# Optimization experiments

Measured on AMD Instinct MI355X. Metric: run time of the kernel, lower is better.

The kernel has to match this reference:

```python
import jax, jax.numpy as jnp
import numpy as np

B, NPG, C = 256, 256, 256  # graphs, nodes-per-graph, in_channels
MAX_LEN = 500


def _sinusoid_pe(max_len, c):
    pos = np.arange(max_len, dtype=np.float32)[:, None]
    div = np.exp(np.arange(0, c, 2, dtype=np.float32) * (-np.log(10000.0) / c))
    pe = np.zeros((max_len, c), np.float32)
    pe[:, 0::2] = np.sin(pos * div)
    pe[:, 1::2] = np.cos(pos * div)
    return jnp.asarray(pe)


def setup_inputs() -> dict:
    key = jax.random.key(0)
    ks = jax.random.split(key, 8)
    N = B * NPG
    x = jax.random.normal(ks[0], (N, C), jnp.float32)
    batch = jnp.repeat(jnp.arange(B, dtype=jnp.int32), NPG)
    # every other atom in each graph is an N/O atom -> 128 per graph
    on_index = (jnp.arange(B, dtype=jnp.int32)[:, None] * NPG
                + jnp.arange(0, NPG, 2, dtype=jnp.int32)[None, :]).reshape(-1)
    W1 = jax.random.normal(ks[1], (C, 256), jnp.float32) / np.sqrt(C)
    b1 = jnp.zeros((256,), jnp.float32)
    W2 = jax.random.normal(ks[2], (256, 128), jnp.float32) / np.sqrt(256.0)
    b2 = jnp.zeros((128,), jnp.float32)
    W3 = jax.random.normal(ks[3], (128, 64), jnp.float32) / np.sqrt(128.0)
    b3 = jnp.zeros((64,), jnp.float32)
    w_atom = jax.random.normal(ks[4], (64,), jnp.float32) / 8.0
    return {"x": x, "pe": _sinusoid_pe(MAX_LEN, C), "W1": W1, "b1": b1,
            "W2": W2, "b2": b2, "W3": W3, "b3": b3, "w_atom": w_atom,
            "batch": batch, "on_index": on_index, "ratio": 16}


def _lrelu(z):
    return jnp.where(z > 0, z, 0.1 * z)


def reference(x, pe, W1, b1, W2, b2, W3, b3, w_atom, batch, on_index, ratio):
    N = x.shape[0]
    bsz = int(batch[-1]) + 1
    num_nodes = jax.ops.segment_sum(jnp.ones_like(batch), batch, num_segments=bsz)
    cum = jnp.concatenate([jnp.zeros((1,), batch.dtype), jnp.cumsum(num_nodes)[:-1]])
    n = int(num_nodes.max())  # max_num_nodes
    idx_in_graph = jnp.arange(N, dtype=batch.dtype) - cum[batch]
    # positional encoding (dropout = identity in eval)
    xp = x + pe[idx_in_graph]
    # scoring MLP
    h = _lrelu(xp @ W1 + b1)
    h = _lrelu(h @ W2 + b2)
    h = _lrelu(h @ W3 + b3)
    score = jnp.tanh((h * w_atom).sum(-1) / jnp.linalg.norm(w_atom))
    # dense-pack scores into [bsz, n] padded with -inf, sort descending per row
    dense_idx = jnp.arange(N, dtype=batch.dtype) - cum[batch] + batch * n
    dense = jnp.full((bsz * n,), jnp.finfo(x.dtype).min, x.dtype).at[dense_idx].set(score)
    order = jnp.argsort(-dense.reshape(bsz, n), axis=-1)       # perm within row
    ranks = jnp.argsort(order, axis=-1)                         # inverse perm
    pos_in_perm = (jnp.arange(bsz)[:, None] * n + ranks).reshape(-1)
    # positions (in the flattened perm) of N/O atoms, sorted -> grouped per graph
    on_par = dense_idx[on_index]                                # padded/parallel ids
    indices = jnp.sort(pos_in_perm[on_par])
    m = on_index.shape[0] // bsz                                # N/O atoms per graph (uniform here)
    k = min(int(ratio), m)                                      # k = min(ratio, on_num)
    pre_mask = (jnp.arange(bsz)[:, None] * m + jnp.arange(k)[None, :]).reshape(-1)
    mask = indices[pre_mask]
    # map padded indices back to global node ids (subtract cumulative void counts)
    void = n - num_nodes
    cum_void = jnp.concatenate([jnp.zeros((1,), batch.dtype), jnp.cumsum(void)[:-1]])
    perm_flat = (order + (jnp.arange(bsz) * n - cum_void)[:, None]).reshape(-1)
    perm = perm_flat[mask]
    x_top = (xp[perm] * score[perm][:, None]).reshape(bsz, int(ratio), -1)
    return (x_top, perm, score[on_index], on_index)
```

## Files before the change

### kernel.cpp

```cpp
#include <hip/hip_runtime.h>
#include <hip/hip_bf16.h>


typedef __attribute__((ext_vector_type(8))) short short8v;
typedef __attribute__((ext_vector_type(4))) float float4v;

#define W1P_OFF 0
#define W2P_OFF 131072
#define W3P_OFF 196608
#define NORM_OFF 212992

static __device__ __forceinline__ float lrelu(float z) { return z > 0.0f ? z : 0.1f * z; }

static __device__ __forceinline__ unsigned f2bfu(float f) {
    union { float f; unsigned u; } v; v.f = f;
    const unsigned r = v.u + 0x7FFFu + ((v.u >> 16) & 1u);
    return r >> 16;
}
static __device__ __forceinline__ short f2bf(float f) { return (short)f2bfu(f); }

static __device__ __forceinline__ int sw_off(int row, int chunk, int within) {
    return row * 256 + ((chunk ^ (row & 7)) << 3) + within;
}

__global__ __launch_bounds__(256) void pack_kernel(
    const float* __restrict__ W1, const float* __restrict__ W2,
    const float* __restrict__ W3, const float* __restrict__ wa,
    short* __restrict__ ws, float* __restrict__ ws_norm)
{
    const int u = blockIdx.x * 256 + threadIdx.x;
    if (u >= 13312) {
        if (u < 13312 + 64) {
            const int l = u - 13312;
            float w = wa[l];
            float p = w * w;
            #pragma unroll
            for (int s = 1; s < 64; s <<= 1) p += __shfl_xor(p, s);
            if (l == 0) ws_norm[0] = sqrtf(p);
        }
        return;
    }
    const float* W; int N, unitBase, uu;
    short* dst;
    if (u < 8192)       { W = W1; N = 256; uu = u;         dst = ws + (W1P_OFF/2); unitBase = 8; }
    else if (u < 12288) { W = W2; N = 128; uu = u - 8192;  dst = ws + (W2P_OFF/2); unitBase = 8; }
    else                { W = W3; N = 64;  uu = u - 12288; dst = ws + (W3P_OFF/2); unitBase = 4; }
    const int perNt = unitBase * 64;
    const int nt   = uu / perNt;
    const int rem  = uu % perNt;
    const int ks   = rem / 64;
    const int lane = rem % 64;
    const int q = lane >> 4;
    const int n = nt * 16 + (lane & 15);
    short8v frag;
    #pragma unroll
    for (int j = 0; j < 8; ++j) {
        const int k = ks * 32 + q * 8 + j;
        frag[j] = f2bf(W[(size_t)k * N + n]);
    }
    *(short8v*)(dst + (size_t)uu * 8) = frag;
}

__global__ __launch_bounds__(1024, 4) void fused_mlp_topk_kernel(
    const float* __restrict__ x, const float* __restrict__ pe,
    const float* __restrict__ b1, const float* __restrict__ b2,
    const float* __restrict__ b3, const float* __restrict__ w_atom,
    const int* __restrict__ on_index, const short* __restrict__ ws_pack,
    const float* __restrict__ ws_norm,
    float* __restrict__ out_perm, float* __restrict__ out_xtop,
    float* __restrict__ out_score, float* __restrict__ out_onidx)
{
    __shared__ __align__(16) short XP[128 * 256];
    __shared__ __align__(16) short H1[128 * 256];
    __shared__ float PART[128][5];
    __shared__ float SC[128];
    __shared__ int   sel_node[16];
    __shared__ float sel_sc[16];

    const int t    = threadIdx.x;
    const int g    = blockIdx.x;
    const int m0   = g * 128;
    const int wid  = t >> 6;
    const int lane = t & 63;
    const int q = lane >> 4;
    const int c = lane & 15;

    const short* W1p = ws_pack + (W1P_OFF / 2);
    const short* W2p = ws_pack + (W2P_OFF / 2);
    const short* W3p = ws_pack + (W3P_OFF / 2);

    #pragma unroll
    for (int i = 0; i < 4; ++i) {
        const int u = t + i * 1024;
        const int r = u >> 5;
        const int ck = u & 31;
        const int k = ck << 3;
        const int node = on_index[m0 + r];
        const float4 xa = *(const float4*)(x + (size_t)node * 256 + k);
        const float4 xb = *(const float4*)(x + (size_t)node * 256 + k + 4);
        const float4 pa = *(const float4*)(pe + (size_t)(node & 255) * 256 + k);
        const float4 pb = *(const float4*)(pe + (size_t)(node & 255) * 256 + k + 4);
        short8v s;
        s[0] = f2bf(xa.x + pa.x); s[1] = f2bf(xa.y + pa.y);
        s[2] = f2bf(xa.z + pa.z); s[3] = f2bf(xa.w + pa.w);
        s[4] = f2bf(xb.x + pb.x); s[5] = f2bf(xb.y + pb.y);
        s[6] = f2bf(xb.z + pb.z); s[7] = f2bf(xb.w + pb.w);
        *(short8v*)(&XP[sw_off(r, ck, 0)]) = s;
    }
    __syncthreads();

    {
        const int mg = wid >> 3;
        const int ng = wid & 7;
        const int r0 = mg * 64;
        float4v acc[2][4];
        #pragma unroll
        for (int gg = 0; gg < 2; ++gg) {
            const float4 bb = *(const float4*)(b1 + (ng * 2 + gg) * 16 + q * 4);
            #pragma unroll
            for (int mt = 0; mt < 4; ++mt)
                acc[gg][mt] = (float4v){bb.x, bb.y, bb.z, bb.w};
        }
        #pragma unroll
        for (int ks = 0; ks < 8; ++ks) {
            const short8v w0 = *(const short8v*)(W1p + ((size_t)((ng * 2 + 0) * 8 + ks) * 64 + lane) * 8);
            const short8v w1 = *(const short8v*)(W1p + ((size_t)((ng * 2 + 1) * 8 + ks) * 64 + lane) * 8);
            #pragma unroll
            for (int mt = 0; mt < 4; ++mt) {
                const short8v a = *(const short8v*)(&XP[sw_off(r0 + mt * 16 + c, ks * 4 + q, 0)]);
                acc[0][mt] = __builtin_amdgcn_mfma_f32_16x16x32_bf16(w0, a, acc[0][mt], 0, 0, 0);
                acc[1][mt] = __builtin_amdgcn_mfma_f32_16x16x32_bf16(w1, a, acc[1][mt], 0, 0, 0);
            }
        }
        #pragma unroll
        for (int gg = 0; gg < 2; ++gg) {
            const int nbase = (ng * 2 + gg) * 16 + q * 4;
            const int chunk = nbase >> 3;
            const int within = nbase & 7;
            #pragma unroll
            for (int mt = 0; mt < 4; ++mt) {
                const int m = r0 + mt * 16 + c;
                uint2 dd;
                dd.x = f2bfu(lrelu(acc[gg][mt][0])) | (f2bfu(lrelu(acc[gg][mt][1])) << 16);
                dd.y = f2bfu(lrelu(acc[gg][mt][2])) | (f2bfu(lrelu(acc[gg][mt][3])) << 16);
                *(uint2*)(&H1[sw_off(m, chunk, within)]) = dd;
            }
        }
    }
    __syncthreads();

    {
        const int mg = wid >> 2;
        const int ng = wid & 3;
        const int r0 = mg * 32;
        float4v acc[2][2];
        #pragma unroll
        for (int gg = 0; gg < 2; ++gg) {
            const float4 bb = *(const float4*)(b2 + (ng * 2 + gg) * 16 + q * 4);
            #pragma unroll
            for (int mt = 0; mt < 2; ++mt)
                acc[gg][mt] = (float4v){bb.x, bb.y, bb.z, bb.w};
        }
        #pragma unroll
        for (int ks = 0; ks < 8; ++ks) {
            const short8v w0 = *(const short8v*)(W2p + ((size_t)((ng * 2 + 0) * 8 + ks) * 64 + lane) * 8);
            const short8v w1 = *(const short8v*)(W2p + ((size_t)((ng * 2 + 1) * 8 + ks) * 64 + lane) * 8);
            #pragma unroll
            for (int mt = 0; mt < 2; ++mt) {
                const short8v a = *(const short8v*)(&H1[sw_off(r0 + mt * 16 + c, ks * 4 + q, 0)]);
                acc[0][mt] = __builtin_amdgcn_mfma_f32_16x16x32_bf16(w0, a, acc[0][mt], 0, 0, 0);
                acc[1][mt] = __builtin_amdgcn_mfma_f32_16x16x32_bf16(w1, a, acc[1][mt], 0, 0, 0);
            }
        }
        #pragma unroll
        for (int gg = 0; gg < 2; ++gg) {
            const int nbase = (ng * 2 + gg) * 16 + q * 4;
            const int chunk = nbase >> 3;
            const int within = nbase & 7;
            #pragma unroll
            for (int mt = 0; mt < 2; ++mt) {
                const int m = r0 + mt * 16 + c;
                uint2 dd;
                dd.x = f2bfu(lrelu(acc[gg][mt][0])) | (f2bfu(lrelu(acc[gg][mt][1])) << 16);
                dd.y = f2bfu(lrelu(acc[gg][mt][2])) | (f2bfu(lrelu(acc[gg][mt][3])) << 16);
                *(uint2*)(&XP[sw_off(m, chunk, within)]) = dd;
            }
        }
    }
    __syncthreads();

    {
        const int nt  = wid & 3;
        const int mt0 = (wid >> 2) * 2;
        float4v acc[2];
        const float4 bb = *(const float4*)(b3 + nt * 16 + q * 4);
        acc[0] = (float4v){bb.x, bb.y, bb.z, bb.w};
        acc[1] = (float4v){bb.x, bb.y, bb.z, bb.w};
        #pragma unroll
        for (int ks = 0; ks < 4; ++ks) {
            const short8v w = *(const short8v*)(W3p + ((size_t)(nt * 4 + ks) * 64 + lane) * 8);
            const short8v a0 = *(const short8v*)(&XP[sw_off((mt0 + 0) * 16 + c, ks * 4 + q, 0)]);
            const short8v a1 = *(const short8v*)(&XP[sw_off((mt0 + 1) * 16 + c, ks * 4 + q, 0)]);
            acc[0] = __builtin_amdgcn_mfma_f32_16x16x32_bf16(w, a0, acc[0], 0, 0, 0);
            acc[1] = __builtin_amdgcn_mfma_f32_16x16x32_bf16(w, a1, acc[1], 0, 0, 0);
        }
        const float4 wv = *(const float4*)(w_atom + nt * 16 + q * 4);
        #pragma unroll
        for (int mt = 0; mt < 2; ++mt) {
            float p = lrelu(acc[mt][0]) * wv.x + lrelu(acc[mt][1]) * wv.y
                    + lrelu(acc[mt][2]) * wv.z + lrelu(acc[mt][3]) * wv.w;
            p += __shfl_xor(p, 16);
            p += __shfl_xor(p, 32);
            if (q == 0) PART[(mt0 + mt) * 16 + c][nt] = p;
        }
    }
    __syncthreads();

    if (t < 128) {
        const float sum = PART[t][0] + PART[t][1] + PART[t][2] + PART[t][3];
        const float sc = tanhf(sum / ws_norm[0]);
        SC[t] = sc;
        out_score[m0 + t] = sc;
        out_onidx[m0 + t] = (float)on_index[m0 + t];
    }
    __syncthreads();

    if (t < 128) {
        const float sj = SC[t];
        int rank = 0;
        for (int i = 0; i < 128; ++i) {
            const float si = SC[i];
            rank += (si > sj) || (si == sj && i < t);
        }
        if (rank < 16) {
            const int node = on_index[m0 + t];
            sel_node[rank] = node;
            sel_sc[rank]   = sj;
            out_perm[g * 16 + rank] = (float)node;
        }
    }
    __syncthreads();

    #pragma unroll
    for (int i = 0; i < 4; ++i) {
        const int idx = t + i * 1024;
        const int k   = idx >> 8;
        const int col = idx & 255;
        const int node = sel_node[k];
        const float sc = sel_sc[k];
        const float v = (x[(size_t)node * 256 + col] + pe[(size_t)(node & 255) * 256 + col]) * sc;
        out_xtop[((size_t)(g * 16 + k)) * 256 + col] = v;
    }
}

extern "C" void kernel_launch(void* const* d_in, const int* in_sizes, int n_in,
                              void* d_out, int out_size, void* d_ws, size_t ws_size,
                              hipStream_t stream)
{
    const float* x   = (const float*)d_in[0];
    const float* pe  = (const float*)d_in[1];
    const float* W1  = (const float*)d_in[2];
    const float* b1  = (const float*)d_in[3];
    const float* W2  = (const float*)d_in[4];
    const float* b2  = (const float*)d_in[5];
    const float* W3  = (const float*)d_in[6];
    const float* b3  = (const float*)d_in[7];
    const float* wa  = (const float*)d_in[8];
    const int* on_index = (const int*)d_in[10];

    float* out = (float*)d_out;
    float* out_xtop  = out;
    float* out_perm  = out + 1048576;
    float* out_score = out + 1048576 + 4096;
    float* out_onidx = out + 1048576 + 4096 + 32768;

    short* ws_pack = (short*)d_ws;
    float* ws_norm = (float*)((char*)d_ws + NORM_OFF);

    hipLaunchKernelGGL(pack_kernel, dim3(53), dim3(256), 0, stream,
                       W1, W2, W3, wa, ws_pack, ws_norm);
    hipLaunchKernelGGL(fused_mlp_topk_kernel, dim3(256), dim3(1024), 0, stream,
                       x, pe, b1, b2, b3, wa, on_index, (const short*)ws_pack,
                       (const float*)ws_norm,
                       out_perm, out_xtop, out_score, out_onidx);
}
```

Baseline: 125.5 us.

## Split input staging to overlap second-half gathers with first-half GEMM; parallelize rank

```diff
diff --git a/kernel.cpp b/kernel.cpp
--- a/kernel.cpp
+++ b/kernel.cpp
@@ -89,24 +89,38 @@
     const short* W2p = ws_pack + (W2P_OFF / 2);
     const short* W3p = ws_pack + (W3P_OFF / 2);
 
-    #pragma unroll
-    for (int i = 0; i < 4; ++i) {
-        const int u = t + i * 1024;
-        const int r = u >> 5;
-        const int ck = u & 31;
-        const int k = ck << 3;
-        const int node = on_index[m0 + r];
-        const float4 xa = *(const float4*)(x + (size_t)node * 256 + k);
-        const float4 xb = *(const float4*)(x + (size_t)node * 256 + k + 4);
-        const float4 pa = *(const float4*)(pe + (size_t)(node & 255) * 256 + k);
-        const float4 pb = *(const float4*)(pe + (size_t)(node & 255) * 256 + k + 4);
-        short8v s;
-        s[0] = f2bf(xa.x + pa.x); s[1] = f2bf(xa.y + pa.y);
-        s[2] = f2bf(xa.z + pa.z); s[3] = f2bf(xa.w + pa.w);
-        s[4] = f2bf(xb.x + pb.x); s[5] = f2bf(xb.y + pb.y);
-        s[6] = f2bf(xb.z + pb.z); s[7] = f2bf(xb.w + pb.w);
-        *(short8v*)(&XP[sw_off(r, ck, 0)]) = s;
-    }
+    const int rA  = t >> 4;
+    const int ckA = t & 15;
+    const int kA  = ckA << 3;
+    {
+        #pragma unroll
+        for (int i = 0; i < 2; ++i) {
+            const int r = rA + i * 64;
+            const int node = on_index[m0 + r];
+            const float4 xa = *(const float4*)(x + (size_t)node * 256 + kA);
+            const float4 xb = *(const float4*)(x + (size_t)node * 256 + kA + 4);
+            const float4 pa = *(const float4*)(pe + (size_t)(node & 255) * 256 + kA);
+            const float4 pb = *(const float4*)(pe + (size_t)(node & 255) * 256 + kA + 4);
+            short8v s;
+            s[0] = f2bf(xa.x + pa.x); s[1] = f2bf(xa.y + pa.y);
+            s[2] = f2bf(xa.z + pa.z); s[3] = f2bf(xa.w + pa.w);
+            s[4] = f2bf(xb.x + pb.x); s[5] = f2bf(xb.y + pb.y);
+            s[6] = f2bf(xb.z + pb.z); s[7] = f2bf(xb.w + pb.w);
+            *(short8v*)(&XP[sw_off(r, ckA, 0)]) = s;
+        }
+    }
+    const int ckB = 16 + (t & 15);
+    const int kB  = ckB << 3;
+    const int node2 = on_index[m0 + rA];
+    const int node3 = on_index[m0 + rA + 64];
+    const float4 xa2 = *(const float4*)(x + (size_t)node2 * 256 + kB);
+    const float4 xb2 = *(const float4*)(x + (size_t)node2 * 256 + kB + 4);
+    const float4 pa2 = *(const float4*)(pe + (size_t)(node2 & 255) * 256 + kB);
+    const float4 pb2 = *(const float4*)(pe + (size_t)(node2 & 255) * 256 + kB + 4);
+    const float4 xa3 = *(const float4*)(x + (size_t)node3 * 256 + kB);
+    const float4 xb3 = *(const float4*)(x + (size_t)node3 * 256 + kB + 4);
+    const float4 pa3 = *(const float4*)(pe + (size_t)(node3 & 255) * 256 + kB);
+    const float4 pb3 = *(const float4*)(pe + (size_t)(node3 & 255) * 256 + kB + 4);
     __syncthreads();
 
     {
@@ -122,7 +136,33 @@
                 acc[gg][mt] = (float4v){bb.x, bb.y, bb.z, bb.w};
         }
         #pragma unroll
-        for (int ks = 0; ks < 8; ++ks) {
+        for (int ks = 0; ks < 4; ++ks) {
+            const short8v w0 = *(const short8v*)(W1p + ((size_t)((ng * 2 + 0) * 8 + ks) * 64 + lane) * 8);
+            const short8v w1 = *(const short8v*)(W1p + ((size_t)((ng * 2 + 1) * 8 + ks) * 64 + lane) * 8);
+            #pragma unroll
+            for (int mt = 0; mt < 4; ++mt) {
+                const short8v a = *(const short8v*)(&XP[sw_off(r0 + mt * 16 + c, ks * 4 + q, 0)]);
+                acc[0][mt] = __builtin_amdgcn_mfma_f32_16x16x32_bf16(w0, a, acc[0][mt], 0, 0, 0);
+                acc[1][mt] = __builtin_amdgcn_mfma_f32_16x16x32_bf16(w1, a, acc[1][mt], 0, 0, 0);
+            }
+        }
+        {
+            short8v s2;
+            s2[0] = f2bf(xa2.x + pa2.x); s2[1] = f2bf(xa2.y + pa2.y);
+            s2[2] = f2bf(xa2.z + pa2.z); s2[3] = f2bf(xa2.w + pa2.w);
+            s2[4] = f2bf(xb2.x + pb2.x); s2[5] = f2bf(xb2.y + pb2.y);
+            s2[6] = f2bf(xb2.z + pb2.z); s2[7] = f2bf(xb2.w + pb2.w);
+            *(short8v*)(&XP[sw_off(rA, ckB, 0)]) = s2;
+            short8v s3;
+            s3[0] = f2bf(xa3.x + pa3.x); s3[1] = f2bf(xa3.y + pa3.y);
+            s3[2] = f2bf(xa3.z + pa3.z); s3[3] = f2bf(xa3.w + pa3.w);
+            s3[4] = f2bf(xb3.x + pb3.x); s3[5] = f2bf(xb3.y + pb3.y);
+            s3[6] = f2bf(xb3.z + pb3.z); s3[7] = f2bf(xb3.w + pb3.w);
+            *(short8v*)(&XP[sw_off(rA + 64, ckB, 0)]) = s3;
+        }
+        __syncthreads();
+        #pragma unroll
+        for (int ks = 4; ks < 8; ++ks) {
             const short8v w0 = *(const short8v*)(W1p + ((size_t)((ng * 2 + 0) * 8 + ks) * 64 + lane) * 8);
             const short8v w1 = *(const short8v*)(W1p + ((size_t)((ng * 2 + 1) * 8 + ks) * 64 + lane) * 8);
             #pragma unroll
@@ -225,15 +265,21 @@
     }
     __syncthreads();
 
-    if (t < 128) {
-        const float sj = SC[t];
+    {
+        const int j = t >> 3, p = t & 7;
+        const float sj = SC[j];
         int rank = 0;
-        for (int i = 0; i < 128; ++i) {
+        #pragma unroll
+        for (int ii = 0; ii < 16; ++ii) {
+            const int i = p * 16 + ii;
             const float si = SC[i];
-            rank += (si > sj) || (si == sj && i < t);
-        }
-        if (rank < 16) {
-            const int node = on_index[m0 + t];
+            rank += (si > sj) || (si == sj && i < j);
+        }
+        rank += __shfl_xor(rank, 1);
+        rank += __shfl_xor(rank, 2);
+        rank += __shfl_xor(rank, 4);
+        if (p == 0 && rank < 16) {
+            const int node = on_index[m0 + j];
             sel_node[rank] = node;
             sel_sc[rank]   = sj;
             out_perm[g * 16 + rank] = (float)node;
```

Measured after the change: 125.1 us. No clear change (-0.4%).
